# Performance work log

Hardware: AMD Instinct MI355X
Metric: run time of the kernel (lower is better)

The kernel has to match this reference:

```python
import jax, jax.numpy as jnp
import numpy as np

WS = 7          # window_size
NH = 12         # num_heads
EPS = 1e-5      # LayerNorm eps


def setup_inputs() -> dict:
    key = jax.random.key(0)
    ks = jax.random.split(key, 8)
    B, H, W, C = 32, 56, 56, 384
    x = jax.random.normal(ks[0], (B, H * W, C), dtype=jnp.float32)
    s = 1.0 / np.sqrt(C)
    return {
        "x": x,
        "ln_gamma": jnp.ones((C,), jnp.float32),
        "ln_beta": jnp.zeros((C,), jnp.float32),
        "w_in": jax.random.normal(ks[1], (3 * C, C), jnp.float32) * s,   # torch in_proj_weight
        "b_in": jnp.zeros((3 * C,), jnp.float32),
        "w_out": jax.random.normal(ks[2], (C, C), jnp.float32) * s,      # torch out_proj.weight
        "b_out": jnp.zeros((C,), jnp.float32),
        "H": H,
        "W": W,
    }


def reference(x, ln_gamma, ln_beta, w_in, b_in, w_out, b_out, H, W):
    B, N, C = x.shape
    assert N == H * W
    hd = C // NH
    shortcut = x

    # LayerNorm
    mu = jnp.mean(x, axis=-1, keepdims=True)
    var = jnp.mean((x - mu) ** 2, axis=-1, keepdims=True)
    y = (x - mu) * jax.lax.rsqrt(var + EPS) * ln_gamma + ln_beta

    # window partition (pads are static Python ints)
    y = y.reshape(B, H, W, C)
    pad_h = (WS - H % WS) % WS
    pad_w = (WS - W % WS) % WS
    y = jnp.pad(y, ((0, 0), (0, pad_h), (0, pad_w), (0, 0)))
    Hp, Wp = H + pad_h, W + pad_w
    nh, nw = Hp // WS, Wp // WS
    y = y.reshape(B, nh, WS, nw, WS, C).transpose(0, 1, 3, 2, 4, 5)
    y = y.reshape(B * nh * nw, WS * WS, C)   # [NWIN, L, C]

    # MHA (torch nn.MultiheadAttention, batch_first)
    qkv = y @ w_in.T + b_in                   # [NWIN, L, 3C]
    q, k, v = jnp.split(qkv, 3, axis=-1)
    NWIN, L, _ = y.shape
    q = q.reshape(NWIN, L, NH, hd).transpose(0, 2, 1, 3)
    k = k.reshape(NWIN, L, NH, hd).transpose(0, 2, 1, 3)
    v = v.reshape(NWIN, L, NH, hd).transpose(0, 2, 1, 3)
    scores = jnp.einsum("whqd,whkd->whqk", q, k) / jnp.sqrt(jnp.float32(hd))
    attn = jax.nn.softmax(scores, axis=-1)
    o = jnp.einsum("whqk,whkd->whqd", attn, v)
    o = o.transpose(0, 2, 1, 3).reshape(NWIN, L, C)
    o = o @ w_out.T + b_out

    # window reverse + unpad + residual
    o = o.reshape(B, nh, nw, WS, WS, C).transpose(0, 1, 3, 2, 4, 5)
    o = o.reshape(B, Hp, Wp, C)[:, :H, :W, :].reshape(B, N, C)
    return shortcut + o
```

## Files before the change

### kernel.cpp

```cpp
#include <hip/hip_runtime.h>

typedef __bf16 bf16x8 __attribute__((ext_vector_type(8)));
typedef float f32x4 __attribute__((ext_vector_type(4)));
typedef unsigned short ushort8 __attribute__((ext_vector_type(8)));

#define LDS_AS(p) ((__attribute__((address_space(3))) void*)(p))
#define GLB_AS(p) ((const __attribute__((address_space(1))) void*)(p))

__device__ __forceinline__ unsigned short f2bf(float f) {
    union { float f; unsigned u; } v; v.f = f;
    unsigned r = v.u + 0x7fffu + ((v.u >> 16) & 1u);
    return (unsigned short)(r >> 16);
}

__global__ __launch_bounds__(256) void convw_kernel(
    const float* __restrict__ wi, const float* __restrict__ wo,
    unsigned short* __restrict__ qw, unsigned short* __restrict__ ow)
{
    const int i = blockIdx.x * 256 + threadIdx.x;
    if (i < 1152 * 384) qw[i] = f2bf(wi[i]);
    if (i < 384 * 384)  ow[i] = f2bf(wo[i]);
}

__global__ __launch_bounds__(256) void ln_kernel(
    const float* __restrict__ x, const float* __restrict__ gam,
    const float* __restrict__ bet, unsigned short* __restrict__ y)
{
    const int lane = threadIdx.x & 63;
    const int wv   = threadIdx.x >> 6;
    const int m    = blockIdx.x * 4 + wv;
    const int win  = m / 49, l = m - win * 49;
    const int b = win >> 6, wh = (win >> 3) & 7, ww = win & 7;
    const int i = l / 7, j = l - i * 7;
    const float2* xr = (const float2*)(x + ((size_t)b * 3136 + (wh * 7 + i) * 56 + (ww * 7 + j)) * 384);

    float2 v[3];
    float s = 0.f, ss = 0.f;
#pragma unroll
    for (int t = 0; t < 3; ++t) {
        v[t] = xr[t * 64 + lane];
        s  += v[t].x + v[t].y;
        ss += v[t].x * v[t].x + v[t].y * v[t].y;
    }
#pragma unroll
    for (int d = 1; d < 64; d <<= 1) {
        s  += __shfl_xor(s, d, 64);
        ss += __shfl_xor(ss, d, 64);
    }
    const float mu  = s * (1.f / 384.f);
    const float var = ss * (1.f / 384.f) - mu * mu;
    const float rs  = rsqrtf(var + 1e-5f);

    unsigned* yr = (unsigned*)(y + (size_t)m * 384);
#pragma unroll
    for (int t = 0; t < 3; ++t) {
        const int c = (t * 64 + lane) * 2;
        float a0 = (v[t].x - mu) * rs * gam[c]     + bet[c];
        float a1 = (v[t].y - mu) * rs * gam[c + 1] + bet[c + 1];
        yr[t * 64 + lane] = (unsigned)f2bf(a0) | ((unsigned)f2bf(a1) << 16);
    }
}

template <int N_, int EPI>
__global__ __launch_bounds__(256) void gemm_kernel(
    const unsigned short* __restrict__ A,
    const unsigned short* __restrict__ Bw,
    const float* __restrict__ bias,
    unsigned short* __restrict__ obf,
    const float* __restrict__ xres,
    float* __restrict__ oflt)
{
    __shared__ unsigned short As[128 * 32];
    __shared__ unsigned short Bs[128 * 32];
    const int lane = threadIdx.x & 63;
    const int wv   = threadIdx.x >> 6;
    const int m0 = blockIdx.y * 128;
    const int n0 = blockIdx.x * 128;
    const int wm = (wv & 1) * 64;
    const int wn = (wv >> 1) * 64;
    const int cl = lane & 15;
    const int qd = lane >> 4;
    const int srow = wv * 16 + (lane >> 2);
    const int scol = (lane & 3) * 8;

    f32x4 acc[4][4] = {};

    for (int kb = 0; kb < 12; ++kb) {
        const int k0 = kb * 32;
        __syncthreads();
#pragma unroll
        for (int t = 0; t < 2; ++t) {
            const unsigned short* ga = A  + (size_t)(m0 + t * 64 + srow) * 384 + k0 + scol;
            __builtin_amdgcn_global_load_lds(GLB_AS(ga), LDS_AS(As + (t * 64 + wv * 16) * 32), 16, 0, 0);
            const unsigned short* gb = Bw + (size_t)(n0 + t * 64 + srow) * 384 + k0 + scol;
            __builtin_amdgcn_global_load_lds(GLB_AS(gb), LDS_AS(Bs + (t * 64 + wv * 16) * 32), 16, 0, 0);
        }
        __syncthreads();

        bf16x8 af[4], bfr[4];
#pragma unroll
        for (int mt = 0; mt < 4; ++mt)
            af[mt] = *(const bf16x8*)(As + (wm + mt * 16 + cl) * 32 + qd * 8);
#pragma unroll
        for (int nt = 0; nt < 4; ++nt)
            bfr[nt] = *(const bf16x8*)(Bs + (wn + nt * 16 + cl) * 32 + qd * 8);
#pragma unroll
        for (int mt = 0; mt < 4; ++mt)
#pragma unroll
            for (int nt = 0; nt < 4; ++nt)
                acc[mt][nt] = __builtin_amdgcn_mfma_f32_16x16x32_bf16(af[mt], bfr[nt], acc[mt][nt], 0, 0, 0);
    }

#pragma unroll
    for (int mt = 0; mt < 4; ++mt) {
#pragma unroll
        for (int nt = 0; nt < 4; ++nt) {
            const int col = n0 + wn + nt * 16 + cl;
            const float bv = bias[col];
#pragma unroll
            for (int r = 0; r < 4; ++r) {
                const int m = m0 + wm + mt * 16 + qd * 4 + r;
                const float val = acc[mt][nt][r] + bv;
                if (EPI == 0) {
                    obf[(size_t)m * N_ + col] = f2bf(val);
                } else {
                    const int win = m / 49, l = m - win * 49;
                    const int b = win >> 6, wh = (win >> 3) & 7, ww = win & 7;
                    const int i = l / 7, j = l - i * 7;
                    const size_t sr = ((size_t)b * 3136 + (wh * 7 + i) * 56 + (ww * 7 + j)) * 384 + col;
                    oflt[sr] = xres[sr] + val;
                }
            }
        }
    }
}

__global__ __launch_bounds__(256) void attn_kernel(
    const unsigned short* __restrict__ qkv, unsigned short* __restrict__ o)
{
    __shared__ unsigned short P[4][64 * 72];
    const int lane = threadIdx.x & 63;
    const int wv   = threadIdx.x >> 6;
    const int cl = lane & 15;
    const int qd = lane >> 4;
    const int g   = blockIdx.x * 4 + wv;
    const int win = g / 12;
    const int h   = g - win * 12;
    const unsigned short* base = qkv + (size_t)win * (49 * 1152);

    bf16x8 aq[4], bk[4];
#pragma unroll
    for (int mt = 0; mt < 4; ++mt) {
        const int l = mt * 16 + cl;
        bf16x8 z = {};
        if (l < 49) z = *(const bf16x8*)(base + (size_t)l * 1152 + h * 32 + qd * 8);
        aq[mt] = z;
    }
#pragma unroll
    for (int nt = 0; nt < 4; ++nt) {
        const int lk = nt * 16 + cl;
        bf16x8 z = {};
        if (lk < 49) z = *(const bf16x8*)(base + (size_t)lk * 1152 + 384 + h * 32 + qd * 8);
        bk[nt] = z;
    }
    f32x4 s[4][4] = {};
#pragma unroll
    for (int mt = 0; mt < 4; ++mt)
#pragma unroll
        for (int nt = 0; nt < 4; ++nt)
            s[mt][nt] = __builtin_amdgcn_mfma_f32_16x16x32_bf16(aq[mt], bk[nt], s[mt][nt], 0, 0, 0);

    const float scale = 0.17677669529663687f;
#pragma unroll
    for (int mt = 0; mt < 4; ++mt)
#pragma unroll
        for (int nt = 0; nt < 4; ++nt)
#pragma unroll
            for (int r = 0; r < 4; ++r) {
                float t = s[mt][nt][r] * scale;
                if (nt * 16 + cl >= 49) t = -1e30f;
                s[mt][nt][r] = t;
            }

#pragma unroll
    for (int mt = 0; mt < 4; ++mt)
#pragma unroll
        for (int r = 0; r < 4; ++r) {
            float mx = fmaxf(fmaxf(s[mt][0][r], s[mt][1][r]), fmaxf(s[mt][2][r], s[mt][3][r]));
            mx = fmaxf(mx, __shfl_xor(mx, 1, 64));
            mx = fmaxf(mx, __shfl_xor(mx, 2, 64));
            mx = fmaxf(mx, __shfl_xor(mx, 4, 64));
            mx = fmaxf(mx, __shfl_xor(mx, 8, 64));
            float sm = 0.f;
#pragma unroll
            for (int nt = 0; nt < 4; ++nt) {
                const float p = __expf(s[mt][nt][r] - mx);
                s[mt][nt][r] = p;
                sm += p;
            }
            sm += __shfl_xor(sm, 1, 64);
            sm += __shfl_xor(sm, 2, 64);
            sm += __shfl_xor(sm, 4, 64);
            sm += __shfl_xor(sm, 8, 64);
            const float inv = 1.f / sm;
#pragma unroll
            for (int nt = 0; nt < 4; ++nt)
                s[mt][nt][r] *= inv;
        }

    unsigned short* Pw = &P[wv][0];
#pragma unroll
    for (int mt = 0; mt < 4; ++mt)
#pragma unroll
        for (int nt = 0; nt < 4; ++nt)
#pragma unroll
            for (int r = 0; r < 4; ++r)
                Pw[(mt * 16 + qd * 4 + r) * 72 + nt * 16 + cl] = f2bf(s[mt][nt][r]);

    f32x4 oa[4][2] = {};
    const unsigned short* vbase = base + 768 + h * 32;
#pragma unroll
    for (int kk = 0; kk < 2; ++kk) {
        bf16x8 ap[4];
#pragma unroll
        for (int mt = 0; mt < 4; ++mt)
            ap[mt] = *(const bf16x8*)(Pw + (mt * 16 + cl) * 72 + kk * 32 + qd * 8);
#pragma unroll
        for (int nt = 0; nt < 2; ++nt) {
            ushort8 tv;
#pragma unroll
            for (int jj = 0; jj < 8; ++jj) {
                const int lk = kk * 32 + qd * 8 + jj;
                tv[jj] = (lk < 49) ? vbase[(size_t)lk * 1152 + nt * 16 + cl] : (unsigned short)0;
            }
            const bf16x8 bv = __builtin_bit_cast(bf16x8, tv);
#pragma unroll
            for (int mt = 0; mt < 4; ++mt)
                oa[mt][nt] = __builtin_amdgcn_mfma_f32_16x16x32_bf16(ap[mt], bv, oa[mt][nt], 0, 0, 0);
        }
    }

    unsigned short* ob = o + (size_t)win * 49 * 384 + h * 32;
#pragma unroll
    for (int mt = 0; mt < 4; ++mt)
#pragma unroll
        for (int r = 0; r < 4; ++r) {
            const int l = mt * 16 + qd * 4 + r;
            if (l < 49) {
#pragma unroll
                for (int nt = 0; nt < 2; ++nt)
                    ob[(size_t)l * 384 + nt * 16 + cl] = f2bf(oa[mt][nt][r]);
            }
        }
}

extern "C" void kernel_launch(void* const* d_in, const int* in_sizes, int n_in,
                              void* d_out, int out_size, void* d_ws, size_t ws_size,
                              hipStream_t stream)
{
    const float* x   = (const float*)d_in[0];
    const float* gam = (const float*)d_in[1];
    const float* bet = (const float*)d_in[2];
    const float* wi  = (const float*)d_in[3];
    const float* bi  = (const float*)d_in[4];
    const float* wo  = (const float*)d_in[5];
    const float* bo  = (const float*)d_in[6];
    float* out = (float*)d_out;

    const int Bb   = in_sizes[0] / (3136 * 384);
    const int M    = Bb * 3136;
    const int NWIN = Bb * 64;

    char* ws = (char*)d_ws;
    unsigned short* qw   = (unsigned short*)(ws);
    unsigned short* ow   = (unsigned short*)(ws + 884736);
    unsigned short* y    = (unsigned short*)(ws + 1179648);
    unsigned short* qkv  = (unsigned short*)(ws + 1179648 + (size_t)M * 768);
    unsigned short* owin = (unsigned short*)(ws + 1179648 + (size_t)M * 768 + (size_t)M * 2304);

    convw_kernel<<<1728, 256, 0, stream>>>(wi, wo, qw, ow);
    ln_kernel<<<M / 4, 256, 0, stream>>>(x, gam, bet, y);
    gemm_kernel<1152, 0><<<dim3(9, M / 128), 256, 0, stream>>>(y, qw, bi, qkv, nullptr, nullptr);
    attn_kernel<<<NWIN * 12 / 4, 256, 0, stream>>>(qkv, owin);
    gemm_kernel<384, 1><<<dim3(3, M / 128), 256, 0, stream>>>(owin, ow, bo, nullptr, x, out);
}
```

Before: 627.0 us.

## Double-buffer GEMM LDS tiles, swizzle block order, vectorize epilogue stores

The GEMM kernel now double-buffers its A/B LDS tiles so the next k-slice's global-to-LDS load is issued before the MFMAs on the current slice, cutting one barrier per iteration. The grid becomes 1D with an XCD-aware block remap. The MFMA operands are swapped, so each lane's accumulator holds 4 consecutive columns, and the epilogue writes them as vector stores (packed bf16 pairs, or float4 with a float4 residual load). The cost is twice the LDS use and the risk of a race on buffer reuse, since only a single barrier remains per iteration.

```diff
diff --git a/kernel.cpp b/kernel.cpp
--- a/kernel.cpp
+++ b/kernel.cpp
@@ -3,6 +3,7 @@
 typedef __bf16 bf16x8 __attribute__((ext_vector_type(8)));
 typedef float f32x4 __attribute__((ext_vector_type(4)));
 typedef unsigned short ushort8 __attribute__((ext_vector_type(8)));
+typedef unsigned int uu2 __attribute__((ext_vector_type(2)));
 
 #define LDS_AS(p) ((__attribute__((address_space(3))) void*)(p))
 #define GLB_AS(p) ((const __attribute__((address_space(1))) void*)(p))
@@ -70,12 +71,19 @@
     const float* __restrict__ xres,
     float* __restrict__ oflt)
 {
-    __shared__ unsigned short As[128 * 32];
-    __shared__ unsigned short Bs[128 * 32];
+    __shared__ unsigned short As[2][128 * 32];
+    __shared__ unsigned short Bs[2][128 * 32];
     const int lane = threadIdx.x & 63;
     const int wv   = threadIdx.x >> 6;
-    const int m0 = blockIdx.y * 128;
-    const int n0 = blockIdx.x * 128;
+
+    const int NB = N_ / 128;
+    int sw = blockIdx.x;
+    if ((gridDim.x & 7) == 0)
+        sw = (sw & 7) * (int)(gridDim.x >> 3) + (sw >> 3);
+    const int my = sw / NB;
+    const int m0 = my * 128;
+    const int n0 = (sw - my * NB) * 128;
+
     const int wm = (wv & 1) * 64;
     const int wn = (wv >> 1) * 64;
     const int cl = lane & 15;
@@ -85,51 +93,67 @@
 
     f32x4 acc[4][4] = {};
 
+#define STAGE(BUF, KB) do {                                                                              \
+    const unsigned short* ga = A  + (size_t)(m0 + srow) * 384 + (KB) * 32 + scol;                        \
+    const unsigned short* gb = Bw + (size_t)(n0 + srow) * 384 + (KB) * 32 + scol;                        \
+    __builtin_amdgcn_global_load_lds(GLB_AS(ga),            LDS_AS(&As[BUF][(wv * 16) * 32]),        16, 0, 0); \
+    __builtin_amdgcn_global_load_lds(GLB_AS(ga + 64 * 384), LDS_AS(&As[BUF][(64 + wv * 16) * 32]),   16, 0, 0); \
+    __builtin_amdgcn_global_load_lds(GLB_AS(gb),            LDS_AS(&Bs[BUF][(wv * 16) * 32]),        16, 0, 0); \
+    __builtin_amdgcn_global_load_lds(GLB_AS(gb + 64 * 384), LDS_AS(&Bs[BUF][(64 + wv * 16) * 32]),   16, 0, 0); \
+  } while (0)
+
+    STAGE(0, 0);
+    __syncthreads();
+
+#pragma unroll
     for (int kb = 0; kb < 12; ++kb) {
-        const int k0 = kb * 32;
+        const int cur = kb & 1;
+        if (kb < 11) STAGE(cur ^ 1, kb + 1);
+
+        bf16x8 af[4], bfr[4];
+#pragma unroll
+        for (int mt = 0; mt < 4; ++mt)
+            af[mt] = *(const bf16x8*)(&As[cur][(wm + mt * 16 + cl) * 32 + qd * 8]);
+#pragma unroll
+        for (int nt = 0; nt < 4; ++nt)
+            bfr[nt] = *(const bf16x8*)(&Bs[cur][(wn + nt * 16 + cl) * 32 + qd * 8]);
+#pragma unroll
+        for (int mt = 0; mt < 4; ++mt)
+#pragma unroll
+            for (int nt = 0; nt < 4; ++nt)
+                acc[mt][nt] = __builtin_amdgcn_mfma_f32_16x16x32_bf16(bfr[nt], af[mt], acc[mt][nt], 0, 0, 0);
+
         __syncthreads();
-#pragma unroll
-        for (int t = 0; t < 2; ++t) {
-            const unsigned short* ga = A  + (size_t)(m0 + t * 64 + srow) * 384 + k0 + scol;
-            __builtin_amdgcn_global_load_lds(GLB_AS(ga), LDS_AS(As + (t * 64 + wv * 16) * 32), 16, 0, 0);
-            const unsigned short* gb = Bw + (size_t)(n0 + t * 64 + srow) * 384 + k0 + scol;
-            __builtin_amdgcn_global_load_lds(GLB_AS(gb), LDS_AS(Bs + (t * 64 + wv * 16) * 32), 16, 0, 0);
-        }
-        __syncthreads();
-
-        bf16x8 af[4], bfr[4];
-#pragma unroll
-        for (int mt = 0; mt < 4; ++mt)
-            af[mt] = *(const bf16x8*)(As + (wm + mt * 16 + cl) * 32 + qd * 8);
-#pragma unroll
-        for (int nt = 0; nt < 4; ++nt)
-            bfr[nt] = *(const bf16x8*)(Bs + (wn + nt * 16 + cl) * 32 + qd * 8);
-#pragma unroll
-        for (int mt = 0; mt < 4; ++mt)
-#pragma unroll
-            for (int nt = 0; nt < 4; ++nt)
-                acc[mt][nt] = __builtin_amdgcn_mfma_f32_16x16x32_bf16(af[mt], bfr[nt], acc[mt][nt], 0, 0, 0);
-    }
+    }
+#undef STAGE
 
 #pragma unroll
     for (int mt = 0; mt < 4; ++mt) {
+        const int m = m0 + wm + mt * 16 + cl;
+        size_t rowbase = 0;
+        if (EPI == 1) {
+            const int win = m / 49, l = m - win * 49;
+            const int b = win >> 6, wh = (win >> 3) & 7, ww = win & 7;
+            const int i = l / 7, j = l - i * 7;
+            rowbase = ((size_t)b * 3136 + (wh * 7 + i) * 56 + (ww * 7 + j)) * 384;
+        }
 #pragma unroll
         for (int nt = 0; nt < 4; ++nt) {
-            const int col = n0 + wn + nt * 16 + cl;
-            const float bv = bias[col];
-#pragma unroll
-            for (int r = 0; r < 4; ++r) {
-                const int m = m0 + wm + mt * 16 + qd * 4 + r;
-                const float val = acc[mt][nt][r] + bv;
-                if (EPI == 0) {
-                    obf[(size_t)m * N_ + col] = f2bf(val);
-                } else {
-                    const int win = m / 49, l = m - win * 49;
-                    const int b = win >> 6, wh = (win >> 3) & 7, ww = win & 7;
-                    const int i = l / 7, j = l - i * 7;
-                    const size_t sr = ((size_t)b * 3136 + (wh * 7 + i) * 56 + (ww * 7 + j)) * 384 + col;
-                    oflt[sr] = xres[sr] + val;
-                }
+            const int nb = n0 + wn + nt * 16 + qd * 4;
+            const f32x4 bv = *(const f32x4*)(bias + nb);
+            if (EPI == 0) {
+                uu2 p;
+                p[0] = (unsigned)f2bf(acc[mt][nt][0] + bv[0]) |
+                       ((unsigned)f2bf(acc[mt][nt][1] + bv[1]) << 16);
+                p[1] = (unsigned)f2bf(acc[mt][nt][2] + bv[2]) |
+                       ((unsigned)f2bf(acc[mt][nt][3] + bv[3]) << 16);
+                *(uu2*)(obf + (size_t)m * N_ + nb) = p;
+            } else {
+                const f32x4 xr = *(const f32x4*)(xres + rowbase + nb);
+                f32x4 o;
+#pragma unroll
+                for (int r = 0; r < 4; ++r) o[r] = acc[mt][nt][r] + bv[r] + xr[r];
+                *(f32x4*)(oflt + rowbase + nb) = o;
             }
         }
     }
@@ -280,7 +304,7 @@
 
     convw_kernel<<<1728, 256, 0, stream>>>(wi, wo, qw, ow);
     ln_kernel<<<M / 4, 256, 0, stream>>>(x, gam, bet, y);
-    gemm_kernel<1152, 0><<<dim3(9, M / 128), 256, 0, stream>>>(y, qw, bi, qkv, nullptr, nullptr);
+    gemm_kernel<1152, 0><<<(M / 128) * 9, 256, 0, stream>>>(y, qw, bi, qkv, nullptr, nullptr);
     attn_kernel<<<NWIN * 12 / 4, 256, 0, stream>>>(qkv, owin);
-    gemm_kernel<384, 1><<<dim3(3, M / 128), 256, 0, stream>>>(owin, ow, bo, nullptr, x, out);
-}
+    gemm_kernel<384, 1><<<(M / 128) * 3, 256, 0, stream>>>(owin, ow, bo, nullptr, x, out);
+}
```

Result: slower. 646.5 us (+3.1%).
